# Kernel tuning notes

Hardware: AMD Instinct MI355X
Metric: run time of the kernel (lower is better)

The kernel has to match this reference:

```python
import jax, jax.numpy as jnp
import numpy as np

TAU = 2.0        # LIF membrane time constant
VTH = 1.0        # spike threshold
VRESET = 0.0     # hard reset voltage
ALPHA = 2.0      # ATan surrogate alpha
LN_EPS = 1e-5


@jax.custom_vjp
def atan_spike(x):
    # Heaviside forward, ATan surrogate backward (spikingjelly surrogate.ATan)
    return (x >= 0.0).astype(x.dtype)

def _atan_fwd(x):
    return atan_spike(x), x

def _atan_bwd(x, g):
    z = (jnp.pi / 2.0) * ALPHA * x
    return (g * (ALPHA / 2.0) / (1.0 + z * z),)

atan_spike.defvjp(_atan_fwd, _atan_bwd)


def layer_norm(x, w, b):
    mu = jnp.mean(x, axis=-1, keepdims=True)
    var = jnp.mean(jnp.square(x - mu), axis=-1, keepdims=True)
    return (x - mu) * jax.lax.rsqrt(var + LN_EPS) * w + b


def time_shift(x):
    # x: [B,T,C] -> x shifted by one step in time, zero-padded at t=0
    return jnp.pad(x, ((0, 0), (1, 0), (0, 0)))[:, :-1]


def wkv(time_decay, time_first, k, v):
    # Numerically-stable RWKV WKV recurrence. k, v: [B,T,C]
    w = -jnp.exp(time_decay)  # [C]
    u = time_first            # [C]
    B, T, C = k.shape
    kT = jnp.moveaxis(k, 1, 0)  # [T,B,C]
    vT = jnp.moveaxis(v, 1, 0)
    init = (jnp.zeros((B, C), k.dtype),
            jnp.zeros((B, C), k.dtype),
            jnp.full((B, C), -1e38, k.dtype))

    def step(carry, kv_t):
        aa, bb, pp = carry
        kt, vt = kv_t
        ww = u + kt
        p = jnp.maximum(pp, ww)
        e1 = jnp.exp(pp - p)
        e2 = jnp.exp(ww - p)
        y = (e1 * aa + e2 * vt) / (e1 * bb + e2)
        ww2 = pp + w
        p2 = jnp.maximum(ww2, kt)
        e1b = jnp.exp(ww2 - p2)
        e2b = jnp.exp(kt - p2)
        return (e1b * aa + e2b * vt, e1b * bb + e2b, p2), y

    _, yT = jax.lax.scan(step, init, (kT, vT))
    return jnp.moveaxis(yT, 0, 1)  # [B,T,C]


def lif(x):
    # MultiStepLIFNode: tau=2, decay_input=True, v_th=1, hard reset to 0.
    # Recurrence runs over the sequence dim (permute(1,0,2) in torch is layout only).
    xT = jnp.moveaxis(x, 1, 0)  # [T,B,C]
    v0 = jnp.zeros_like(xT[0])

    def step(v, xt):
        v = v + (xt - (v - VRESET)) / TAU
        s = atan_spike(v - VTH)
        v = (1.0 - s) * v + s * VRESET
        return v, s

    _, sT = jax.lax.scan(step, v0, xT)
    return jnp.moveaxis(sT, 0, 1)


def rwkv_time_mix(x, time_decay, time_first, mix_k, mix_v, mix_r, Wk, Wv, Wr, Wo):
    xx = time_shift(x)
    xk = x * mix_k + xx * (1.0 - mix_k)
    xv = x * mix_v + xx * (1.0 - mix_v)
    xr = x * mix_r + xx * (1.0 - mix_r)
    k = jnp.einsum('btc,cd->btd', xk, Wk)
    v = jnp.einsum('btc,cd->btd', xv, Wv)
    r = jax.nn.sigmoid(jnp.einsum('btc,cd->btd', xr, Wr))
    y = wkv(time_decay, time_first, k, v)
    return jnp.einsum('btc,cd->btd', r * y, Wo)


def rwkv_channel_mix(x, mix_k, mix_r, Wk, Wv, Wr):
    xx = time_shift(x)
    xk = x * mix_k + xx * (1.0 - mix_k)
    xr = x * mix_r + xx * (1.0 - mix_r)
    k = jnp.square(jax.nn.relu(jnp.einsum('btc,ch->bth', xk, Wk)))  # relu^2
    kv = jnp.einsum('bth,hc->btc', k, Wv)
    return jax.nn.sigmoid(jnp.einsum('btc,cd->btd', xr, Wr)) * kv


def setup_inputs() -> dict:
    key = jax.random.key(0)
    B, T, C, H = 8, 2048, 768, 3072
    ks = jax.random.split(key, 20)
    p = lambda k, shape, s=0.02: (jax.random.normal(k, shape, jnp.float32) * s)
    u = lambda k, shape: jax.random.uniform(k, shape, jnp.float32)
    return {
        'x': jax.random.normal(ks[0], (B, T, C), jnp.float32),
        'ln1_w': jnp.ones((C,), jnp.float32), 'ln1_b': jnp.zeros((C,), jnp.float32),
        'ln2_w': jnp.ones((C,), jnp.float32), 'ln2_b': jnp.zeros((C,), jnp.float32),
        'att_time_decay': p(ks[1], (C,), 1.0),
        'att_time_first': p(ks[2], (C,), 1.0),
        'att_mix_k': u(ks[3], (C,)), 'att_mix_v': u(ks[4], (C,)), 'att_mix_r': u(ks[5], (C,)),
        'att_Wk': p(ks[6], (C, C)), 'att_Wv': p(ks[7], (C, C)),
        'att_Wr': p(ks[8], (C, C)), 'att_Wo': p(ks[9], (C, C)),
        'ffn_mix_k': u(ks[10], (C,)), 'ffn_mix_r': u(ks[11], (C,)),
        'ffn_Wk': p(ks[12], (C, H)), 'ffn_Wv': p(ks[13], (H, C)), 'ffn_Wr': p(ks[14], (C, C)),
    }


def reference(x, ln1_w, ln1_b, ln2_w, ln2_b,
              att_time_decay, att_time_first, att_mix_k, att_mix_v, att_mix_r,
              att_Wk, att_Wv, att_Wr, att_Wo,
              ffn_mix_k, ffn_mix_r, ffn_Wk, ffn_Wv, ffn_Wr):
    # Block.forward with layer_id != 0 (no ln0, att path); dropout in eval mode.
    a = rwkv_time_mix(layer_norm(x, ln1_w, ln1_b), att_time_decay, att_time_first,
                      att_mix_k, att_mix_v, att_mix_r, att_Wk, att_Wv, att_Wr, att_Wo)
    x = x + lif(a)
    f = rwkv_channel_mix(layer_norm(x, ln2_w, ln2_b), ffn_mix_k, ffn_mix_r,
                         ffn_Wk, ffn_Wv, ffn_Wr)
    x = x + lif(f)
    return x
```

## Files before the change

kernel.cpp:

```cpp
#include <hip/hip_runtime.h>

#define B_ 8
#define T_ 2048
#define C_ 768
#define H_ 3072
#define BT_ (B_ * T_)
#define BC_ (B_ * C_)
#define WSEG 128
#define NWSEG 16
#define LSEG 128
#define NLSEG 16
#define LWARM 96

typedef unsigned short u16;
typedef short bf16x8 __attribute__((ext_vector_type(8)));
typedef float f32x4 __attribute__((ext_vector_type(4)));

__device__ __forceinline__ float b2f(u16 u) {
    union { unsigned i; float f; } w; w.i = ((unsigned)u) << 16; return w.f;
}
__device__ __forceinline__ u16 f2b(float f) {
    union { float f; unsigned i; } w; w.f = f;
    return (u16)((w.i + 0x7fffu + ((w.i >> 16) & 1u)) >> 16);
}

typedef __attribute__((address_space(3))) unsigned int lds_u32;
typedef const __attribute__((address_space(1))) unsigned int glb_u32;
__device__ __forceinline__ void gld_lds16(const void* g, void* l) {
    __builtin_amdgcn_global_load_lds((glb_u32*)g, (lds_u32*)l, 16, 0, 0);
}

template<int NOUT>
__global__ void lnmix(const float* __restrict__ x, const float* __restrict__ w,
                      const float* __restrict__ b,
                      const float* __restrict__ m1, const float* __restrict__ m2,
                      const float* __restrict__ m3,
                      u16* __restrict__ o1, u16* __restrict__ o2, u16* __restrict__ o3) {
    int row = blockIdx.x;
    int t = row % T_;
    const float* xr = x + (size_t)row * C_;
    const float* xp = xr - C_;
    int tid = threadIdx.x;
    float s = 0.f, s2 = 0.f, ps = 0.f, ps2 = 0.f;
    for (int i = tid; i < C_; i += 256) {
        float v = xr[i]; s += v; s2 += v * v;
        if (t > 0) { float u = xp[i]; ps += u; ps2 += u * u; }
    }
    for (int off = 32; off > 0; off >>= 1) {
        s += __shfl_down(s, off);  s2 += __shfl_down(s2, off);
        ps += __shfl_down(ps, off); ps2 += __shfl_down(ps2, off);
    }
    __shared__ float red[4][4];
    int wid = tid >> 6, lane = tid & 63;
    if (lane == 0) { red[wid][0] = s; red[wid][1] = s2; red[wid][2] = ps; red[wid][3] = ps2; }
    __syncthreads();
    if (tid == 0) {
        float a0 = 0, a1 = 0, a2 = 0, a3 = 0;
        for (int i = 0; i < 4; ++i) { a0 += red[i][0]; a1 += red[i][1]; a2 += red[i][2]; a3 += red[i][3]; }
        red[0][0] = a0; red[0][1] = a1; red[0][2] = a2; red[0][3] = a3;
    }
    __syncthreads();
    float mu = red[0][0] * (1.f / C_);
    float rs = rsqrtf(red[0][1] * (1.f / C_) - mu * mu + 1e-5f);
    float pmu = red[0][2] * (1.f / C_);
    float prs = rsqrtf(red[0][3] * (1.f / C_) - pmu * pmu + 1e-5f);
    size_t ob = (size_t)row * C_;
    for (int i = tid; i < C_; i += 256) {
        float wi = w[i], bi = b[i];
        float n = (xr[i] - mu) * rs * wi + bi;
        float np = (t > 0) ? (xp[i] - pmu) * prs * wi + bi : 0.f;
        o1[ob + i] = f2b(fmaf(m1[i], n - np, np));
        o2[ob + i] = f2b(fmaf(m2[i], n - np, np));
        if constexpr (NOUT == 3) o3[ob + i] = f2b(fmaf(m3[i], n - np, np));
    }
}

struct TCJ { const float* s; u16* d; int R, Ncol, nbx, b0; };
struct TC7 { TCJ j[7]; };
__global__ void tcast_all(TC7 jobs) {
    __shared__ float t[32][33];
    int bid = blockIdx.x;
    int ji = 0;
#pragma unroll
    for (int k = 1; k < 7; ++k) if (bid >= jobs.j[k].b0) ji = k;
    TCJ jb = jobs.j[ji];
    int local = bid - jb.b0;
    int bx = local % jb.nbx, by = local / jb.nbx;
    int c0 = bx * 32, r0 = by * 32;
    int col = threadIdx.x & 31, rw = threadIdx.x >> 5;
#pragma unroll
    for (int i = 0; i < 4; ++i) {
        int r = rw + i * 8;
        t[r][col] = jb.s[(size_t)(r0 + r) * jb.Ncol + c0 + col];
    }
    __syncthreads();
#pragma unroll
    for (int i = 0; i < 4; ++i) {
        int r = rw + i * 8;
        jb.d[(size_t)(c0 + r) * jb.R + r0 + col] = f2b(t[col][r]);
    }
}

__device__ __forceinline__ void gemm_core(const u16* __restrict__ A,
                                          const u16* __restrict__ WT,
                                          int K, int m0, int n0,
                                          u16* As, u16* Bs, f32x4 acc[4][8]) {
    const int tid = threadIdx.x;
    const int lane = tid & 63, wid = tid >> 6;
    const int wr = wid >> 1, wc = wid & 1;
    const int r16 = lane & 15, g = lane >> 4;

    const int srow = tid >> 2;
    const int sslot = tid & 3;
    const int sx = (srow >> 1) & 3;
    const u16* gA0 = A + (size_t)(m0 + srow) * K + ((sslot ^ sx) << 3);
    const u16* gA1 = gA0 + (size_t)64 * K;
    const u16* gB0 = WT + (size_t)(n0 + srow) * K + ((sslot ^ sx) << 3);
    const u16* gB1 = gB0 + (size_t)64 * K;
    const u16* gB2 = gB0 + (size_t)128 * K;
    const u16* gB3 = gB0 + (size_t)192 * K;
    u16* lA = As + tid * 8;
    u16* lB = Bs + tid * 8;

    int offA[4], offB[8];
#pragma unroll
    for (int m = 0; m < 4; ++m) {
        int row = wr * 64 + m * 16 + r16;
        offA[m] = row * 32 + (g ^ ((row >> 1) & 3)) * 8;
    }
#pragma unroll
    for (int n = 0; n < 8; ++n) {
        int rob = wc * 128 + n * 16 + r16;
        offB[n] = rob * 32 + (g ^ ((rob >> 1) & 3)) * 8;
    }

#define STAGE6(ao, bo) do { \
        gld_lds16(gA0, lA + (ao));        gld_lds16(gA1, lA + (ao) + 2048); \
        gld_lds16(gB0, lB + (bo));        gld_lds16(gB1, lB + (bo) + 2048); \
        gld_lds16(gB2, lB + (bo) + 4096); gld_lds16(gB3, lB + (bo) + 6144); \
        gA0 += 32; gA1 += 32; gB0 += 32; gB1 += 32; gB2 += 32; gB3 += 32; } while (0)

    const int nk = K >> 5;
    STAGE6(0, 0);
    STAGE6(4096, 8192);
    asm volatile("s_waitcnt vmcnt(6)" ::: "memory");
    __builtin_amdgcn_s_barrier();
    int wA = 8192, wB = 16384;
    int rA = 0, rB = 0;

    for (int kt = 0; kt < nk; ++kt) {
        const u16* Ab = As + rA;
        const u16* Bb = Bs + rB;
        bf16x8 af[4], bg[8];
#pragma unroll
        for (int m = 0; m < 4; ++m) af[m] = *(const bf16x8*)(Ab + offA[m]);
#pragma unroll
        for (int n = 0; n < 8; ++n) bg[n] = *(const bf16x8*)(Bb + offB[n]);
        __builtin_amdgcn_sched_barrier(0);
        if (kt + 2 < nk) {
            STAGE6(wA, wB);
            wA += 4096; if (wA == 12288) wA = 0;
            wB += 8192; if (wB == 24576) wB = 0;
        }
        asm volatile("s_waitcnt lgkmcnt(0)" ::: "memory");
        __builtin_amdgcn_sched_barrier(0);
        __builtin_amdgcn_s_setprio(1);
#pragma unroll
        for (int m = 0; m < 4; ++m)
#pragma unroll
            for (int n = 0; n < 8; ++n)
                acc[m][n] = __builtin_amdgcn_mfma_f32_16x16x32_bf16(af[m], bg[n], acc[m][n], 0, 0, 0);
        __builtin_amdgcn_s_setprio(0);
        __builtin_amdgcn_sched_barrier(0);
        if (kt + 1 < nk) {
            if (kt + 2 < nk) asm volatile("s_waitcnt vmcnt(6)" ::: "memory");
            else             asm volatile("s_waitcnt vmcnt(0)" ::: "memory");
            __builtin_amdgcn_sched_barrier(0);
            __builtin_amdgcn_s_barrier();
        }
        rA += 4096; if (rA == 12288) rA = 0;
        rB += 8192; if (rB == 24576) rB = 0;
    }
#undef STAGE6
}

__device__ __forceinline__ void xcd_remap2(int& bx, int& by) {
    const int gx = gridDim.x;
    const int nwg = gx * gridDim.y;
    const int lin = blockIdx.y * gx + blockIdx.x;
    const int q = nwg >> 3, r = nwg & 7;
    const int xcd = lin & 7, pos = lin >> 3;
    const int nid = (xcd < r ? xcd * (q + 1) : r * (q + 1) + (xcd - r) * q) + pos;
    bx = nid % gx;
    by = nid / gx;
}

template<int MODE, bool EMUL>
__global__ __launch_bounds__(256, 2)
void gemm2(const u16* __restrict__ A, const u16* __restrict__ WT,
           u16* __restrict__ Cout, const u16* __restrict__ Emul, int N, int K) {
    __shared__ u16 As[12288];
    __shared__ u16 Bs[24576];
    int bx, by;
    xcd_remap2(bx, by);
    const int m0 = by << 7, n0 = bx << 8;
    f32x4 acc[4][8];
#pragma unroll
    for (int i = 0; i < 4; ++i)
#pragma unroll
        for (int j = 0; j < 8; ++j)
#pragma unroll
            for (int q = 0; q < 4; ++q) acc[i][j][q] = 0.f;
    gemm_core(A, WT, K, m0, n0, As, Bs, acc);

    const int lane = threadIdx.x & 63, wid = threadIdx.x >> 6;
    const int wr = wid >> 1, wc = wid & 1;
    const int r16 = lane & 15, g = lane >> 4;
#pragma unroll
    for (int m = 0; m < 4; ++m)
#pragma unroll
        for (int n = 0; n < 8; ++n)
#pragma unroll
            for (int j = 0; j < 4; ++j) {
                int row = m0 + wr * 64 + m * 16 + g * 4 + j;
                int col = n0 + wc * 128 + n * 16 + r16;
                float v = acc[m][n][j];
                if constexpr (MODE == 1) v = 1.f / (1.f + expf(-v));
                if constexpr (MODE == 2) { v = fmaxf(v, 0.f); v = v * v; }
                size_t o = (size_t)row * N + col;
                if constexpr (EMUL) v *= b2f(Emul[o]);
                Cout[o] = f2b(v);
            }
}

struct P3 {
    const u16 *A0, *A1, *A2;
    const u16 *W0, *W1, *W2;
    u16 *O0, *O1, *O2;
};
__global__ __launch_bounds__(256, 2)
void proj3(P3 p, int N, int K) {
    __shared__ u16 As[12288];
    __shared__ u16 Bs[24576];
    const int z = blockIdx.z;
    const u16* A = (z == 0) ? p.A0 : (z == 1) ? p.A1 : p.A2;
    const u16* W = (z == 0) ? p.W0 : (z == 1) ? p.W1 : p.W2;
    u16* O = (z == 0) ? p.O0 : (z == 1) ? p.O1 : p.O2;
    int bx, by;
    xcd_remap2(bx, by);
    const int m0 = by << 7, n0 = bx << 8;
    f32x4 acc[4][8];
#pragma unroll
    for (int i = 0; i < 4; ++i)
#pragma unroll
        for (int j = 0; j < 8; ++j)
#pragma unroll
            for (int q = 0; q < 4; ++q) acc[i][j][q] = 0.f;
    gemm_core(A, W, K, m0, n0, As, Bs, acc);

    const int lane = threadIdx.x & 63, wid = threadIdx.x >> 6;
    const int wr = wid >> 1, wc = wid & 1;
    const int r16 = lane & 15, g = lane >> 4;
    const bool sig = (z == 2);
#pragma unroll
    for (int m = 0; m < 4; ++m)
#pragma unroll
        for (int n = 0; n < 8; ++n)
#pragma unroll
            for (int j = 0; j < 4; ++j) {
                int row = m0 + wr * 64 + m * 16 + g * 4 + j;
                int col = n0 + wc * 128 + n * 16 + r16;
                float v = acc[m][n][j];
                if (sig) v = 1.f / (1.f + expf(-v));
                O[(size_t)row * N + col] = f2b(v);
            }
}

struct J2 {
    const u16 *A0, *W0; u16 *O0;
    const u16 *A1, *W1; u16 *O1;
};
__global__ __launch_bounds__(256, 2)
void ffn1rr(J2 p, int K) {
    __shared__ u16 As[12288];
    __shared__ u16 Bs[24576];
    int bx, by;
    xcd_remap2(bx, by);
    const bool isF = (bx < 12);
    const u16* A = isF ? p.A0 : p.A1;
    const u16* W = isF ? p.W0 : p.W1;
    u16* O = isF ? p.O0 : p.O1;
    const int N = isF ? 3072 : 768;
    const int m0 = by << 7;
    const int n0 = (isF ? bx : bx - 12) << 8;
    f32x4 acc[4][8];
#pragma unroll
    for (int i = 0; i < 4; ++i)
#pragma unroll
        for (int j = 0; j < 8; ++j)
#pragma unroll
            for (int q = 0; q < 4; ++q) acc[i][j][q] = 0.f;
    gemm_core(A, W, K, m0, n0, As, Bs, acc);

    const int lane = threadIdx.x & 63, wid = threadIdx.x >> 6;
    const int wr = wid >> 1, wc = wid & 1;
    const int r16 = lane & 15, g = lane >> 4;
#pragma unroll
    for (int m = 0; m < 4; ++m)
#pragma unroll
        for (int n = 0; n < 8; ++n)
#pragma unroll
            for (int j = 0; j < 4; ++j) {
                int row = m0 + wr * 64 + m * 16 + g * 4 + j;
                int col = n0 + wc * 128 + n * 16 + r16;
                float v = acc[m][n][j];
                if (isF) { v = fmaxf(v, 0.f); v = v * v; }
                else     { v = 1.f / (1.f + expf(-v)); }
                O[(size_t)row * N + col] = f2b(v);
            }
}

__global__ void wkv_p1(const float* __restrict__ td, const u16* __restrict__ K,
                       const u16* __restrict__ V, float* __restrict__ st) {
    int bc = blockIdx.x * 256 + threadIdx.x;
    int seg = blockIdx.y;
    int b = bc / C_, c = bc - b * C_;
    float w = -expf(td[c]);
    size_t off = (size_t)b * T_ * C_ + (size_t)seg * WSEG * C_ + c;
    float aa = 0.f, bb = 0.f, pp = -1e38f;
#pragma unroll 4
    for (int i = 0; i < WSEG; ++i) {
        float kt = b2f(K[off + (size_t)i * C_]);
        float vt = b2f(V[off + (size_t)i * C_]);
        float ww2 = pp + w;
        float p2 = fmaxf(ww2, kt);
        float e1 = expf(ww2 - p2);
        float e2 = expf(kt - p2);
        aa = e1 * aa + e2 * vt;
        bb = e1 * bb + e2;
        pp = p2;
    }
    int sidx = seg * 3 * BC_ + bc;
    st[sidx] = aa; st[sidx + BC_] = bb; st[sidx + 2 * BC_] = pp;
}

__global__ void wkv_p2(const float* __restrict__ td, const float* __restrict__ st,
                       float* __restrict__ ini) {
    int bc = blockIdx.x * 256 + threadIdx.x;
    int c = bc % C_;
    float wL = -expf(td[c]) * (float)WSEG;
    float aa = 0.f, bb = 0.f, pp = -1e38f;
    for (int s = 0; s < NWSEG; ++s) {
        int sidx = s * 3 * BC_ + bc;
        ini[sidx] = aa; ini[sidx + BC_] = bb; ini[sidx + 2 * BC_] = pp;
        float la = st[sidx], lb = st[sidx + BC_], lp = st[sidx + 2 * BC_];
        float ppw = pp + wL;
        float p = fmaxf(ppw, lp);
        float e1 = expf(ppw - p), e2 = expf(lp - p);
        aa = e1 * aa + e2 * la;
        bb = e1 * bb + e2 * lb;
        pp = p;
    }
}

__global__ void wkv_p3(const float* __restrict__ td, const float* __restrict__ tf,
                       const u16* __restrict__ K, const u16* __restrict__ V,
                       const u16* __restrict__ R, const float* __restrict__ ini,
                       u16* __restrict__ RY) {
    int bc = blockIdx.x * 256 + threadIdx.x;
    int seg = blockIdx.y;
    int b = bc / C_, c = bc - b * C_;
    float w = -expf(td[c]);
    float u = tf[c];
    int sidx = seg * 3 * BC_ + bc;
    float aa = ini[sidx], bb = ini[sidx + BC_], pp = ini[sidx + 2 * BC_];
    size_t off = (size_t)b * T_ * C_ + (size_t)seg * WSEG * C_ + c;
#pragma unroll 4
    for (int i = 0; i < WSEG; ++i) {
        float kt = b2f(K[off + (size_t)i * C_]);
        float vt = b2f(V[off + (size_t)i * C_]);
        float rr = b2f(R[off + (size_t)i * C_]);
        float ww = u + kt;
        float p = fmaxf(pp, ww);
        float e1 = expf(pp - p);
        float e2 = expf(ww - p);
        RY[off + (size_t)i * C_] = f2b(rr * (e1 * aa + e2 * vt) / (e1 * bb + e2));
        float ww2 = pp + w;
        float p2 = fmaxf(ww2, kt);
        float e1b = expf(ww2 - p2);
        float e2b = expf(kt - p2);
        aa = e1b * aa + e2b * vt;
        bb = e1b * bb + e2b;
        pp = p2;
    }
}

__global__ void lif_add_b(const u16* __restrict__ cur, const float* __restrict__ base,
                          float* __restrict__ out) {
    int bc = blockIdx.x * 256 + threadIdx.x;
    int seg = blockIdx.y;
    int b = bc / C_, c = bc - b * C_;
    size_t rowbase = (size_t)b * T_ * C_ + c;
    int t0 = seg * LSEG;
    int tw = t0 - LWARM; if (tw < 0) tw = 0;
    int nw = t0 - tw;
    float v = 0.f;
    const u16* cp = cur + rowbase + (size_t)tw * C_;
#pragma unroll 8
    for (int i = 0; i < nw; ++i) {
        float xt = b2f(cp[(size_t)i * C_]);
        v += (xt - v) * 0.5f;
        v = (v >= 1.f) ? 0.f : v;
    }
    const u16* c2 = cur + rowbase + (size_t)t0 * C_;
    const float* bp = base + rowbase + (size_t)t0 * C_;
    float* op = out + rowbase + (size_t)t0 * C_;
#pragma unroll 8
    for (int i = 0; i < LSEG; ++i) {
        float xt = b2f(c2[(size_t)i * C_]);
        v += (xt - v) * 0.5f;
        float sp = (v >= 1.f) ? 1.f : 0.f;
        op[(size_t)i * C_] = bp[(size_t)i * C_] + sp;
        v = (sp > 0.f) ? 0.f : v;
    }
}

extern "C" void kernel_launch(void* const* d_in, const int* in_sizes, int n_in,
                              void* d_out, int out_size, void* d_ws, size_t ws_size,
                              hipStream_t stream) {
    const float* x    = (const float*)d_in[0];
    const float* ln1w = (const float*)d_in[1];
    const float* ln1b = (const float*)d_in[2];
    const float* ln2w = (const float*)d_in[3];
    const float* ln2b = (const float*)d_in[4];
    const float* td   = (const float*)d_in[5];
    const float* tf   = (const float*)d_in[6];
    const float* amk  = (const float*)d_in[7];
    const float* amv  = (const float*)d_in[8];
    const float* amr  = (const float*)d_in[9];
    const float* aWk  = (const float*)d_in[10];
    const float* aWv  = (const float*)d_in[11];
    const float* aWr  = (const float*)d_in[12];
    const float* aWo  = (const float*)d_in[13];
    const float* fmk  = (const float*)d_in[14];
    const float* fmr  = (const float*)d_in[15];
    const float* fWk  = (const float*)d_in[16];
    const float* fWv  = (const float*)d_in[17];
    const float* fWr  = (const float*)d_in[18];
    float* out = (float*)d_out;

    const size_t NBC = (size_t)BT_ * C_;
    u16* WkT = (u16*)d_ws;
    u16* WvT = WkT + 589824;
    u16* WrT = WvT + 589824;
    u16* WoT = WrT + 589824;
    u16* FrT = WoT + 589824;
    u16* FkT = FrT + 589824;
    u16* FvT = FkT + 2359296;
    float* st  = (float*)(FvT + 2359296);
    float* ini = st + NWSEG * 3 * BC_;
    u16* S0 = (u16*)(ini + NWSEG * 3 * BC_);
    u16* S1 = S0 + NBC;
    u16* S2 = S1 + NBC;
    u16* S3 = S2 + NBC;
    u16* Hbuf = S3 + NBC;
    size_t fixed_b = (size_t)((char*)Hbuf - (char*)d_ws);

    int NCH = 4;
    if (ws_size >= fixed_b + ((size_t)BT_ * H_ + NBC) * 2) NCH = 1;
    else if (ws_size >= fixed_b + ((size_t)(BT_ / 2) * H_ + NBC / 2) * 2) NCH = 2;
    const int CH = BT_ / NCH;
    u16* Fbuf = Hbuf + (size_t)CH * H_;

    u16* Kb = (u16*)d_out;
    u16* Vb = Kb + NBC;

    {
        TC7 jobs;
        const float* srcs[7] = {aWk, aWv, aWr, aWo, fWr, fWk, fWv};
        u16* dsts[7] = {WkT, WvT, WrT, WoT, FrT, FkT, FvT};
        int Rs[7]    = {768, 768, 768, 768, 768, 768, 3072};
        int Ns[7]    = {768, 768, 768, 768, 768, 3072, 768};
        int b0 = 0;
        for (int k = 0; k < 7; ++k) {
            jobs.j[k].s = srcs[k]; jobs.j[k].d = dsts[k];
            jobs.j[k].R = Rs[k]; jobs.j[k].Ncol = Ns[k];
            jobs.j[k].nbx = Ns[k] / 32; jobs.j[k].b0 = b0;
            b0 += (Ns[k] / 32) * (Rs[k] / 32);
        }
        tcast_all<<<b0, 256, 0, stream>>>(jobs);
    }

    lnmix<3><<<BT_, 256, 0, stream>>>(x, ln1w, ln1b, amk, amv, amr, S0, S1, S2);
    {
        P3 p{S0, S1, S2, WkT, WvT, WrT, Kb, Vb, S3};
        proj3<<<dim3(3, 128, 3), 256, 0, stream>>>(p, C_, C_);
    }
    wkv_p1<<<dim3(BC_ / 256, NWSEG), 256, 0, stream>>>(td, Kb, Vb, st);
    wkv_p2<<<BC_ / 256, 256, 0, stream>>>(td, st, ini);
    wkv_p3<<<dim3(BC_ / 256, NWSEG), 256, 0, stream>>>(td, tf, Kb, Vb, S3, ini, S0);
    gemm2<0, false><<<dim3(3, 128), 256, 0, stream>>>(S0, WoT, S1, nullptr, C_, C_);
    lif_add_b<<<dim3(BC_ / 256, NLSEG), 256, 0, stream>>>(S1, x, out);
    lnmix<2><<<BT_, 256, 0, stream>>>(out, ln2w, ln2b, fmk, fmr, nullptr, S0, S1, nullptr);

    if (NCH == 1) {
        J2 p{S0, FkT, Hbuf, S1, FrT, S2};
        ffn1rr<<<dim3(15, 128), 256, 0, stream>>>(p, C_);
        gemm2<0, true><<<dim3(3, 128), 256, 0, stream>>>(Hbuf, FvT, Fbuf, S2, C_, H_);
        lif_add_b<<<dim3(BC_ / 256, NLSEG), 256, 0, stream>>>(Fbuf, out, out);
    } else {
        gemm2<1, false><<<dim3(3, 128), 256, 0, stream>>>(S1, FrT, S2, nullptr, C_, C_);
        for (int ch = 0; ch < NCH; ++ch) {
            const u16* xk2c = S0 + (size_t)ch * CH * C_;
            const u16* rrc  = S2 + (size_t)ch * CH * C_;
            gemm2<2, false><<<dim3(12, CH / 128), 256, 0, stream>>>(xk2c, FkT, Hbuf, nullptr, H_, C_);
            gemm2<0, true><<<dim3(3, CH / 128), 256, 0, stream>>>(Hbuf, FvT, Fbuf, rrc, C_, H_);
            lif_add_b<<<dim3((CH / T_) * C_ / 256, NLSEG), 256, 0, stream>>>(
                Fbuf, out + (size_t)ch * CH * C_, out + (size_t)ch * CH * C_);
        }
    }
}
```

Measured before the change: 579.5 us.

## Switch GEMMs to 256x256 tiles with 512 threads and split-phase pipelining

Replaces the 128x256 tile, 256-thread GEMM core with a 256x256 tile computed by 8 waves. Each K-step is split into two MFMA halves, with A and B global-to-LDS staging interleaved between them across a triple-buffered shared tile. The goal is more operand reuse per LDS byte and better overlap of loads with MFMA. In exchange, occupancy drops to one block per CU with 96KB of LDS, grids halve (e.g. 192 blocks for the N=768 GEMMs, fewer than the CU count), and each step carries extra barriers.

```diff
diff --git a/kernel.cpp b/kernel.cpp
--- a/kernel.cpp
+++ b/kernel.cpp
@@ -101,87 +101,103 @@
     }
 }
 
-__device__ __forceinline__ void gemm_core(const u16* __restrict__ A,
-                                          const u16* __restrict__ WT,
-                                          int K, int m0, int n0,
-                                          u16* As, u16* Bs, f32x4 acc[4][8]) {
+__device__ __forceinline__ void gemm_core256(const u16* __restrict__ A,
+                                             const u16* __restrict__ WT,
+                                             int K, int m0, int n0,
+                                             u16* L, f32x4 acc[8][4]) {
     const int tid = threadIdx.x;
     const int lane = tid & 63, wid = tid >> 6;
-    const int wr = wid >> 1, wc = wid & 1;
+    const int wr = wid >> 2, wc = wid & 3;
     const int r16 = lane & 15, g = lane >> 4;
 
     const int srow = tid >> 2;
-    const int sslot = tid & 3;
+    const int sunit = tid & 3;
     const int sx = (srow >> 1) & 3;
-    const u16* gA0 = A + (size_t)(m0 + srow) * K + ((sslot ^ sx) << 3);
-    const u16* gA1 = gA0 + (size_t)64 * K;
-    const u16* gB0 = WT + (size_t)(n0 + srow) * K + ((sslot ^ sx) << 3);
-    const u16* gB1 = gB0 + (size_t)64 * K;
-    const u16* gB2 = gB0 + (size_t)128 * K;
-    const u16* gB3 = gB0 + (size_t)192 * K;
-    u16* lA = As + tid * 8;
-    u16* lB = Bs + tid * 8;
-
-    int offA[4], offB[8];
-#pragma unroll
-    for (int m = 0; m < 4; ++m) {
-        int row = wr * 64 + m * 16 + r16;
+    const u16* gA0 = A + (size_t)(m0 + srow) * K + ((sunit ^ sx) << 3);
+    const u16* gA1 = gA0 + (size_t)128 * K;
+    const u16* gB0 = WT + (size_t)(n0 + srow) * K + ((sunit ^ sx) << 3);
+    const u16* gB1 = gB0 + (size_t)128 * K;
+    u16* lA0 = L + tid * 8;
+    u16* lA1 = L + 4096 + tid * 8;
+    u16* lB0 = L + 8192 + tid * 8;
+    u16* lB1 = L + 12288 + tid * 8;
+
+    int offA[8], offB[4];
+#pragma unroll
+    for (int m = 0; m < 8; ++m) {
+        int row = wr * 128 + m * 16 + r16;
         offA[m] = row * 32 + (g ^ ((row >> 1) & 3)) * 8;
     }
 #pragma unroll
-    for (int n = 0; n < 8; ++n) {
-        int rob = wc * 128 + n * 16 + r16;
-        offB[n] = rob * 32 + (g ^ ((rob >> 1) & 3)) * 8;
-    }
-
-#define STAGE6(ao, bo) do { \
-        gld_lds16(gA0, lA + (ao));        gld_lds16(gA1, lA + (ao) + 2048); \
-        gld_lds16(gB0, lB + (bo));        gld_lds16(gB1, lB + (bo) + 2048); \
-        gld_lds16(gB2, lB + (bo) + 4096); gld_lds16(gB3, lB + (bo) + 6144); \
-        gA0 += 32; gA1 += 32; gB0 += 32; gB1 += 32; gB2 += 32; gB3 += 32; } while (0)
-
-    const int nk = K >> 5;
-    STAGE6(0, 0);
-    STAGE6(4096, 8192);
-    asm volatile("s_waitcnt vmcnt(6)" ::: "memory");
+    for (int n = 0; n < 4; ++n) {
+        int rob = wc * 64 + n * 16 + r16;
+        offB[n] = 8192 + rob * 32 + (g ^ ((rob >> 1) & 3)) * 8;
+    }
+
+#define STGA(buf) do { \
+        gld_lds16(gA0, lA0 + (buf) * 16384); gld_lds16(gA1, lA1 + (buf) * 16384); \
+        gA0 += 32; gA1 += 32; } while (0)
+#define STGB(buf) do { \
+        gld_lds16(gB0, lB0 + (buf) * 16384); gld_lds16(gB1, lB1 + (buf) * 16384); \
+        gB0 += 32; gB1 += 32; } while (0)
+
+    const int nt = K >> 5;
+    STGA(0); STGB(0);
+    STGA(1); STGB(1);
+    asm volatile("s_waitcnt vmcnt(4)" ::: "memory");
+    __builtin_amdgcn_sched_barrier(0);
     __builtin_amdgcn_s_barrier();
-    int wA = 8192, wB = 16384;
-    int rA = 0, rB = 0;
-
-    for (int kt = 0; kt < nk; ++kt) {
-        const u16* Ab = As + rA;
-        const u16* Bb = Bs + rB;
-        bf16x8 af[4], bg[8];
-#pragma unroll
-        for (int m = 0; m < 4; ++m) af[m] = *(const bf16x8*)(Ab + offA[m]);
-#pragma unroll
-        for (int n = 0; n < 8; ++n) bg[n] = *(const bf16x8*)(Bb + offB[n]);
+
+    int rb = 0, wb = 2;
+    for (int t = 0; t < nt; ++t) {
+        const u16* Lb = L + rb * 16384;
+        const bool stg = (t + 2 < nt);
+        bf16x8 a0[4], bg[4];
+#pragma unroll
+        for (int m = 0; m < 4; ++m) a0[m] = *(const bf16x8*)(Lb + offA[m]);
+#pragma unroll
+        for (int n = 0; n < 4; ++n) bg[n] = *(const bf16x8*)(Lb + offB[n]);
         __builtin_amdgcn_sched_barrier(0);
-        if (kt + 2 < nk) {
-            STAGE6(wA, wB);
-            wA += 4096; if (wA == 12288) wA = 0;
-            wB += 8192; if (wB == 24576) wB = 0;
-        }
+        if (stg) STGA(wb);
+        __builtin_amdgcn_s_barrier();
         asm volatile("s_waitcnt lgkmcnt(0)" ::: "memory");
         __builtin_amdgcn_sched_barrier(0);
         __builtin_amdgcn_s_setprio(1);
 #pragma unroll
         for (int m = 0; m < 4; ++m)
 #pragma unroll
-            for (int n = 0; n < 8; ++n)
-                acc[m][n] = __builtin_amdgcn_mfma_f32_16x16x32_bf16(af[m], bg[n], acc[m][n], 0, 0, 0);
+            for (int n = 0; n < 4; ++n)
+                acc[m][n] = __builtin_amdgcn_mfma_f32_16x16x32_bf16(a0[m], bg[n], acc[m][n], 0, 0, 0);
         __builtin_amdgcn_s_setprio(0);
         __builtin_amdgcn_sched_barrier(0);
-        if (kt + 1 < nk) {
-            if (kt + 2 < nk) asm volatile("s_waitcnt vmcnt(6)" ::: "memory");
-            else             asm volatile("s_waitcnt vmcnt(0)" ::: "memory");
+        __builtin_amdgcn_s_barrier();
+        bf16x8 a1[4];
+#pragma unroll
+        for (int m = 0; m < 4; ++m) a1[m] = *(const bf16x8*)(Lb + offA[4 + m]);
+        __builtin_amdgcn_sched_barrier(0);
+        if (stg) STGB(wb);
+        __builtin_amdgcn_s_barrier();
+        asm volatile("s_waitcnt lgkmcnt(0)" ::: "memory");
+        __builtin_amdgcn_sched_barrier(0);
+        __builtin_amdgcn_s_setprio(1);
+#pragma unroll
+        for (int m = 0; m < 4; ++m)
+#pragma unroll
+            for (int n = 0; n < 4; ++n)
+                acc[4 + m][n] = __builtin_amdgcn_mfma_f32_16x16x32_bf16(a1[m], bg[n], acc[4 + m][n], 0, 0, 0);
+        __builtin_amdgcn_s_setprio(0);
+        __builtin_amdgcn_sched_barrier(0);
+        if (t + 1 < nt) {
+            if (stg) asm volatile("s_waitcnt vmcnt(4)" ::: "memory");
+            else     asm volatile("s_waitcnt vmcnt(0)" ::: "memory");
             __builtin_amdgcn_sched_barrier(0);
             __builtin_amdgcn_s_barrier();
         }
-        rA += 4096; if (rA == 12288) rA = 0;
-        rB += 8192; if (rB == 24576) rB = 0;
-    }
-#undef STAGE6
+        rb = (rb == 2) ? 0 : rb + 1;
+        wb = (wb == 2) ? 0 : wb + 1;
+    }
+#undef STGA
+#undef STGB
 }
 
 __device__ __forceinline__ void xcd_remap2(int& bx, int& by) {
@@ -195,42 +211,45 @@
     by = nid / gx;
 }
 
+__device__ __forceinline__ void epilogue256(f32x4 acc[8][4], u16* O, const u16* Emul,
+                                            int m0, int n0, int N, int mode, bool emul) {
+    const int lane = threadIdx.x & 63, wid = threadIdx.x >> 6;
+    const int wr = wid >> 2, wc = wid & 3;
+    const int r16 = lane & 15, g = lane >> 4;
+#pragma unroll
+    for (int m = 0; m < 8; ++m)
+#pragma unroll
+        for (int n = 0; n < 4; ++n)
+#pragma unroll
+            for (int j = 0; j < 4; ++j) {
+                int row = m0 + wr * 128 + m * 16 + g * 4 + j;
+                int col = n0 + wc * 64 + n * 16 + r16;
+                float v = acc[m][n][j];
+                if (mode == 1) v = 1.f / (1.f + expf(-v));
+                else if (mode == 2) { v = fmaxf(v, 0.f); v = v * v; }
+                size_t o = (size_t)row * N + col;
+                if (emul) v *= b2f(Emul[o]);
+                O[o] = f2b(v);
+            }
+}
+
 template<int MODE, bool EMUL>
-__global__ __launch_bounds__(256, 2)
-void gemm2(const u16* __restrict__ A, const u16* __restrict__ WT,
-           u16* __restrict__ Cout, const u16* __restrict__ Emul, int N, int K) {
-    __shared__ u16 As[12288];
-    __shared__ u16 Bs[24576];
+__global__ __launch_bounds__(512, 1)
+void gemm256(const u16* __restrict__ A, const u16* __restrict__ WT,
+             u16* __restrict__ Cout, const u16* __restrict__ Emul, int N, int K) {
+    __shared__ u16 L[49152];
     int bx, by;
     xcd_remap2(bx, by);
-    const int m0 = by << 7, n0 = bx << 8;
-    f32x4 acc[4][8];
-#pragma unroll
-    for (int i = 0; i < 4; ++i)
-#pragma unroll
-        for (int j = 0; j < 8; ++j)
+    const int m0 = by << 8, n0 = bx << 8;
+    f32x4 acc[8][4];
+#pragma unroll
+    for (int i = 0; i < 8; ++i)
+#pragma unroll
+        for (int j = 0; j < 4; ++j)
 #pragma unroll
             for (int q = 0; q < 4; ++q) acc[i][j][q] = 0.f;
-    gemm_core(A, WT, K, m0, n0, As, Bs, acc);
-
-    const int lane = threadIdx.x & 63, wid = threadIdx.x >> 6;
-    const int wr = wid >> 1, wc = wid & 1;
-    const int r16 = lane & 15, g = lane >> 4;
-#pragma unroll
-    for (int m = 0; m < 4; ++m)
-#pragma unroll
-        for (int n = 0; n < 8; ++n)
-#pragma unroll
-            for (int j = 0; j < 4; ++j) {
-                int row = m0 + wr * 64 + m * 16 + g * 4 + j;
-                int col = n0 + wc * 128 + n * 16 + r16;
-                float v = acc[m][n][j];
-                if constexpr (MODE == 1) v = 1.f / (1.f + expf(-v));
-                if constexpr (MODE == 2) { v = fmaxf(v, 0.f); v = v * v; }
-                size_t o = (size_t)row * N + col;
-                if constexpr (EMUL) v *= b2f(Emul[o]);
-                Cout[o] = f2b(v);
-            }
+    gemm_core256(A, WT, K, m0, n0, L, acc);
+    epilogue256(acc, Cout, Emul, m0, n0, N, MODE, EMUL);
 }
 
 struct P3 {
@@ -238,52 +257,34 @@
     const u16 *W0, *W1, *W2;
     u16 *O0, *O1, *O2;
 };
-__global__ __launch_bounds__(256, 2)
+__global__ __launch_bounds__(512, 1)
 void proj3(P3 p, int N, int K) {
-    __shared__ u16 As[12288];
-    __shared__ u16 Bs[24576];
+    __shared__ u16 L[49152];
     const int z = blockIdx.z;
     const u16* A = (z == 0) ? p.A0 : (z == 1) ? p.A1 : p.A2;
     const u16* W = (z == 0) ? p.W0 : (z == 1) ? p.W1 : p.W2;
     u16* O = (z == 0) ? p.O0 : (z == 1) ? p.O1 : p.O2;
     int bx, by;
     xcd_remap2(bx, by);
-    const int m0 = by << 7, n0 = bx << 8;
-    f32x4 acc[4][8];
-#pragma unroll
-    for (int i = 0; i < 4; ++i)
-#pragma unroll
-        for (int j = 0; j < 8; ++j)
+    const int m0 = by << 8, n0 = bx << 8;
+    f32x4 acc[8][4];
+#pragma unroll
+    for (int i = 0; i < 8; ++i)
+#pragma unroll
+        for (int j = 0; j < 4; ++j)
 #pragma unroll
             for (int q = 0; q < 4; ++q) acc[i][j][q] = 0.f;
-    gemm_core(A, W, K, m0, n0, As, Bs, acc);
-
-    const int lane = threadIdx.x & 63, wid = threadIdx.x >> 6;
-    const int wr = wid >> 1, wc = wid & 1;
-    const int r16 = lane & 15, g = lane >> 4;
-    const bool sig = (z == 2);
-#pragma unroll
-    for (int m = 0; m < 4; ++m)
-#pragma unroll
-        for (int n = 0; n < 8; ++n)
-#pragma unroll
-            for (int j = 0; j < 4; ++j) {
-                int row = m0 + wr * 64 + m * 16 + g * 4 + j;
-                int col = n0 + wc * 128 + n * 16 + r16;
-                float v = acc[m][n][j];
-                if (sig) v = 1.f / (1.f + expf(-v));
-                O[(size_t)row * N + col] = f2b(v);
-            }
+    gemm_core256(A, W, K, m0, n0, L, acc);
+    epilogue256(acc, O, nullptr, m0, n0, N, (z == 2) ? 1 : 0, false);
 }
 
 struct J2 {
     const u16 *A0, *W0; u16 *O0;
     const u16 *A1, *W1; u16 *O1;
 };
-__global__ __launch_bounds__(256, 2)
+__global__ __launch_bounds__(512, 1)
 void ffn1rr(J2 p, int K) {
-    __shared__ u16 As[12288];
-    __shared__ u16 Bs[24576];
+    __shared__ u16 L[49152];
     int bx, by;
     xcd_remap2(bx, by);
     const bool isF = (bx < 12);
@@ -291,33 +292,17 @@
     const u16* W = isF ? p.W0 : p.W1;
     u16* O = isF ? p.O0 : p.O1;
     const int N = isF ? 3072 : 768;
-    const int m0 = by << 7;
+    const int m0 = by << 8;
     const int n0 = (isF ? bx : bx - 12) << 8;
-    f32x4 acc[4][8];
-#pragma unroll
-    for (int i = 0; i < 4; ++i)
-#pragma unroll
-        for (int j = 0; j < 8; ++j)
+    f32x4 acc[8][4];
+#pragma unroll
+    for (int i = 0; i < 8; ++i)
+#pragma unroll
+        for (int j = 0; j < 4; ++j)
 #pragma unroll
             for (int q = 0; q < 4; ++q) acc[i][j][q] = 0.f;
-    gemm_core(A, W, K, m0, n0, As, Bs, acc);
-
-    const int lane = threadIdx.x & 63, wid = threadIdx.x >> 6;
-    const int wr = wid >> 1, wc = wid & 1;
-    const int r16 = lane & 15, g = lane >> 4;
-#pragma unroll
-    for (int m = 0; m < 4; ++m)
-#pragma unroll
-        for (int n = 0; n < 8; ++n)
-#pragma unroll
-            for (int j = 0; j < 4; ++j) {
-                int row = m0 + wr * 64 + m * 16 + g * 4 + j;
-                int col = n0 + wc * 128 + n * 16 + r16;
-                float v = acc[m][n][j];
-                if (isF) { v = fmaxf(v, 0.f); v = v * v; }
-                else     { v = 1.f / (1.f + expf(-v)); }
-                O[(size_t)row * N + col] = f2b(v);
-            }
+    gemm_core256(A, W, K, m0, n0, L, acc);
+    epilogue256(acc, O, nullptr, m0, n0, N, isF ? 2 : 1, false);
 }
 
 __global__ void wkv_p1(const float* __restrict__ td, const u16* __restrict__ K,
@@ -494,27 +479,27 @@
     lnmix<3><<<BT_, 256, 0, stream>>>(x, ln1w, ln1b, amk, amv, amr, S0, S1, S2);
     {
         P3 p{S0, S1, S2, WkT, WvT, WrT, Kb, Vb, S3};
-        proj3<<<dim3(3, 128, 3), 256, 0, stream>>>(p, C_, C_);
+        proj3<<<dim3(3, 64, 3), 512, 0, stream>>>(p, C_, C_);
     }
     wkv_p1<<<dim3(BC_ / 256, NWSEG), 256, 0, stream>>>(td, Kb, Vb, st);
     wkv_p2<<<BC_ / 256, 256, 0, stream>>>(td, st, ini);
     wkv_p3<<<dim3(BC_ / 256, NWSEG), 256, 0, stream>>>(td, tf, Kb, Vb, S3, ini, S0);
-    gemm2<0, false><<<dim3(3, 128), 256, 0, stream>>>(S0, WoT, S1, nullptr, C_, C_);
+    gemm256<0, false><<<dim3(3, 64), 512, 0, stream>>>(S0, WoT, S1, nullptr, C_, C_);
     lif_add_b<<<dim3(BC_ / 256, NLSEG), 256, 0, stream>>>(S1, x, out);
     lnmix<2><<<BT_, 256, 0, stream>>>(out, ln2w, ln2b, fmk, fmr, nullptr, S0, S1, nullptr);
 
     if (NCH == 1) {
         J2 p{S0, FkT, Hbuf, S1, FrT, S2};
-        ffn1rr<<<dim3(15, 128), 256, 0, stream>>>(p, C_);
-        gemm2<0, true><<<dim3(3, 128), 256, 0, stream>>>(Hbuf, FvT, Fbuf, S2, C_, H_);
+        ffn1rr<<<dim3(15, 64), 512, 0, stream>>>(p, C_);
+        gemm256<0, true><<<dim3(3, 64), 512, 0, stream>>>(Hbuf, FvT, Fbuf, S2, C_, H_);
         lif_add_b<<<dim3(BC_ / 256, NLSEG), 256, 0, stream>>>(Fbuf, out, out);
     } else {
-        gemm2<1, false><<<dim3(3, 128), 256, 0, stream>>>(S1, FrT, S2, nullptr, C_, C_);
+        gemm256<1, false><<<dim3(3, 64), 512, 0, stream>>>(S1, FrT, S2, nullptr, C_, C_);
         for (int ch = 0; ch < NCH; ++ch) {
             const u16* xk2c = S0 + (size_t)ch * CH * C_;
             const u16* rrc  = S2 + (size_t)ch * CH * C_;
-            gemm2<2, false><<<dim3(12, CH / 128), 256, 0, stream>>>(xk2c, FkT, Hbuf, nullptr, H_, C_);
-            gemm2<0, true><<<dim3(3, CH / 128), 256, 0, stream>>>(Hbuf, FvT, Fbuf, rrc, C_, H_);
+            gemm256<2, false><<<dim3(12, CH / 256), 512, 0, stream>>>(xk2c, FkT, Hbuf, nullptr, H_, C_);
+            gemm256<0, true><<<dim3(3, CH / 256), 512, 0, stream>>>(Hbuf, FvT, Fbuf, rrc, C_, H_);
             lif_add_b<<<dim3((CH / T_) * C_ / 256, NLSEG), 256, 0, stream>>>(
                 Fbuf, out + (size_t)ch * CH * C_, out + (size_t)ch * CH * C_);
         }
```

New measurement: 597.3 us. 3.1% more time.
